# Kernel tuning notes

Hardware: AMD Instinct MI355X
Metric: run time of the kernel (lower is better)

Reference implementation:

```python
import jax, jax.numpy as jnp
import numpy as np

EMBED = 1024
HEADS = 16
HEAD_DIM = EMBED // HEADS
B, S = 2, 2048


def setup_inputs() -> dict:
    key = jax.random.key(0)
    ks = jax.random.split(key, 13)
    def lin(kw, kb):
        # torch nn.Linear default init: U(-1/sqrt(fan_in), 1/sqrt(fan_in))
        bound = 1.0 / np.sqrt(EMBED)
        W = jax.random.uniform(kw, (EMBED, EMBED), jnp.float32, -bound, bound)
        b = jax.random.uniform(kb, (EMBED,), jnp.float32, -bound, bound)
        return W, b
    Wq, bq = lin(ks[0], ks[1])
    Wk, bk = lin(ks[2], ks[3])
    Wv, bv = lin(ks[4], ks[5])
    Wo, bo = lin(ks[6], ks[7])
    return {
        "query": jax.random.normal(ks[8], (B, S, EMBED), jnp.float32),
        "key": jax.random.normal(ks[9], (B, S, EMBED), jnp.float32),
        "value": jax.random.normal(ks[10], (B, S, EMBED), jnp.float32),
        "mask": jax.random.randint(ks[11], (B, S, S), 0, 2, jnp.int32),
        "Wq": Wq, "bq": bq, "Wk": Wk, "bk": bk,
        "Wv": Wv, "bv": bv, "Wo": Wo, "bo": bo,
    }


def _split_heads(x):
    b, s, _ = x.shape
    return x.reshape(b, s, HEADS, HEAD_DIM).transpose(0, 2, 1, 3)  # [B,H,S,D]


def reference(query, key, value, mask, Wq, bq, Wk, bk, Wv, bv, Wo, bo):
    scaling = HEAD_DIM ** -0.5
    q = _split_heads(query @ Wq.T + bq) * scaling          # [B,H,Sq,D]
    k = _split_heads(key @ Wk.T + bk)                       # [B,H,Sk,D]
    v = _split_heads(value @ Wv.T + bv)                     # [B,H,Sk,D]
    scores = jnp.einsum('bhqd,bhkd->bhqk', q, k)            # [B,H,Sq,Sk]
    scores = jnp.where(mask[:, None, :, :] == 0, jnp.float32(-10000.0), scores)
    p = jax.nn.softmax(scores, axis=-1)
    x = jnp.einsum('bhqk,bhkd->bhqd', p, v)                 # [B,H,Sq,D]
    b, h, s, d = x.shape
    x = x.transpose(0, 2, 1, 3).reshape(b, s, h * d)
    return x @ Wo.T + bo
```

## Files before the change

kernel.cpp:

```cpp
#include <hip/hip_runtime.h>

#define EMBED 1024
#define HEADS 16
#define HDIM  64
#define BATCH 2
#define SEQ   2048
#define MTOT  (BATCH*SEQ)
#define LOG2E 1.4426950408889634f
#define QSCALE (0.125f * LOG2E)

typedef __attribute__((ext_vector_type(8)))  short short8;
typedef __attribute__((ext_vector_type(4)))  float f32x4;
typedef __attribute__((ext_vector_type(16))) float f32x16;

#define MFMA(a,b,c)   __builtin_amdgcn_mfma_f32_16x16x32_bf16(a,b,c,0,0,0)
#define MFMA32(a,b,c) __builtin_amdgcn_mfma_f32_32x32x16_bf16(a,b,c,0,0,0)

__device__ __forceinline__ ushort f2bf(float f) {
  union { float f; unsigned u; } v; v.f = f;
  unsigned u = v.u;
  unsigned r = u + 0x7fffu + ((u >> 16) & 1u);
  return (ushort)(r >> 16);
}
__device__ __forceinline__ unsigned packbf(float a, float b) {
  return (unsigned)f2bf(a) | ((unsigned)f2bf(b) << 16);
}
__device__ __forceinline__ unsigned cvtpk(float lo, float hi) {
  unsigned r;
  asm("v_cvt_pk_bf16_f32 %0, %1, %2" : "=v"(r) : "v"(lo), "v"(hi));
  return r;
}
__device__ __forceinline__ uint2 cvt4(float4 v) {
  uint2 r;
  asm("v_cvt_pk_bf16_f32 %0, %2, %3\n\t"
      "v_cvt_pk_bf16_f32 %1, %4, %5"
      : "=&v"(r.x), "=&v"(r.y)
      : "v"(v.x), "v"(v.y), "v"(v.z), "v"(v.w));
  return r;
}
__device__ __forceinline__ void gl_lds16(const ushort* g, ushort* l) {
  __builtin_amdgcn_global_load_lds(
      (const __attribute__((address_space(1))) unsigned*)g,
      (__attribute__((address_space(3))) unsigned*)l, 16, 0, 0);
}

__global__ __launch_bounds__(256) void prep(
    const float* __restrict__ s0, const float* __restrict__ s1, const float* __restrict__ s2,
    const float* __restrict__ s3, const float* __restrict__ s4, const float* __restrict__ s5,
    const float* __restrict__ s6, const int* __restrict__ mask,
    ushort* __restrict__ d0, ushort* __restrict__ d1, ushort* __restrict__ d2,
    ushort* __restrict__ d3, ushort* __restrict__ d4, ushort* __restrict__ d5,
    ushort* __restrict__ d6, ushort* __restrict__ mbits16)
{
  const int z = blockIdx.z;
  if (z == 7) {
    size_t i16 = ((size_t)blockIdx.x * 256 + threadIdx.x);
    if (i16 >= (size_t)BATCH * SEQ * SEQ / 16) return;
    const int4* m4 = reinterpret_cast<const int4*>(mask + i16 * 16);
    unsigned bits = 0;
    #pragma unroll
    for (int k = 0; k < 4; ++k) {
      int4 v = m4[k];
      bits |= (unsigned)(v.x != 0) << (4 * k);
      bits |= (unsigned)(v.y != 0) << (4 * k + 1);
      bits |= (unsigned)(v.z != 0) << (4 * k + 2);
      bits |= (unsigned)(v.w != 0) << (4 * k + 3);
    }
    mbits16[i16] = (ushort)bits;
    return;
  }
  const float* s; ushort* d;
  switch (z) {
    case 0: s = s0; d = d0; break;
    case 1: s = s1; d = d1; break;
    case 2: s = s2; d = d2; break;
    case 3: s = s3; d = d3; break;
    case 4: s = s4; d = d4; break;
    case 5: s = s5; d = d5; break;
    default: s = s6; d = d6; break;
  }
  const int nch = (z < 3) ? (MTOT * EMBED / 8) : (EMBED * EMBED / 8);
  int i = blockIdx.x * 256 + threadIdx.x;
  if (i >= nch) return;
  float4 a = reinterpret_cast<const float4*>(s)[2 * i];
  float4 b = reinterpret_cast<const float4*>(s)[2 * i + 1];
  uint2 lo = cvt4(a), hi = cvt4(b);
  reinterpret_cast<uint4*>(d)[i] = make_uint4(lo.x, lo.y, hi.x, hi.y);
}

__global__ __launch_bounds__(512, 6) void gemm_qkv32(
    const ushort* __restrict__ A0, const ushort* __restrict__ A1, const ushort* __restrict__ A2,
    const ushort* __restrict__ W0, const ushort* __restrict__ W1, const ushort* __restrict__ W2,
    const float* __restrict__ b0, const float* __restrict__ b1, const float* __restrict__ b2,
    ushort* __restrict__ oq, ushort* __restrict__ ok, ushort* __restrict__ ov)
{
  __shared__ __align__(16) ushort lds[2][2][4096];

  const int nwg = 768;
  int lin = blockIdx.x + (blockIdx.y << 3);
  int swz = (lin & 7) * (nwg >> 3) + (lin >> 3);
  const int z  = swz >> 8;
  const int r_ = swz & 255;
  const int n0 = (r_ & 7) << 7;
  const int m0 = (r_ >> 3) << 7;

  const ushort* __restrict__ A    = (z == 0) ? A0 : (z == 1) ? A1 : A2;
  const ushort* __restrict__ W    = (z == 0) ? W0 : (z == 1) ? W1 : W2;
  const float*  __restrict__ bias = (z == 0) ? b0 : (z == 1) ? b1 : b2;

  const int t = threadIdx.x;
  const int lane = t & 63;
  const int wid = t >> 6;
  const int wr = wid >> 2, wc = wid & 3;
  const int lr = lane & 15, qg = lane >> 4;

  const int srow = t >> 2;
  const int scol = ((((t & 3) - (srow >> 1)) & 3)) << 3;
  auto stage = [&](int buf, int k0) {
    gl_lds16(&A[(size_t)(m0 + srow) * EMBED + k0 + scol], &lds[buf][0][t * 8]);
    gl_lds16(&W[(size_t)(n0 + srow) * EMBED + k0 + scol], &lds[buf][1][t * 8]);
  };

  f32x4 acc[4][2] = {};

  stage(0, 0);
  asm volatile("s_waitcnt vmcnt(0)" ::: "memory");
  __syncthreads();

  for (int kt = 0; kt < 32; ++kt) {
    const int buf = kt & 1;
    if (kt < 31) stage(buf ^ 1, (kt + 1) * 32);

    short8 af[4], bfr[2];
    #pragma unroll
    for (int mi = 0; mi < 4; ++mi) {
      int row = wr * 64 + mi * 16 + lr;
      int sidx = (qg + (row >> 1)) & 3;
      af[mi] = *reinterpret_cast<const short8*>(&lds[buf][0][row * 32 + (sidx << 3)]);
    }
    #pragma unroll
    for (int ni = 0; ni < 2; ++ni) {
      int row = wc * 32 + ni * 16 + lr;
      int sidx = (qg + (row >> 1)) & 3;
      bfr[ni] = *reinterpret_cast<const short8*>(&lds[buf][1][row * 32 + (sidx << 3)]);
    }
    __builtin_amdgcn_s_setprio(1);
    #pragma unroll
    for (int mi = 0; mi < 4; ++mi)
      #pragma unroll
      for (int ni = 0; ni < 2; ++ni)
        acc[mi][ni] = MFMA(af[mi], bfr[ni], acc[mi][ni]);
    __builtin_amdgcn_s_setprio(0);

    if (kt < 31) {
      asm volatile("s_waitcnt vmcnt(0)" ::: "memory");
      __syncthreads();
    }
  }

  #pragma unroll
  for (int ni = 0; ni < 2; ++ni) {
    int ng = n0 + wc * 32 + ni * 16 + lr;
    float bv_ = bias[ng];
    int h = ng >> 6, d = ng & 63;
    #pragma unroll
    for (int mi = 0; mi < 4; ++mi) {
      #pragma unroll
      for (int r = 0; r < 4; ++r) {
        int mg = m0 + wr * 64 + mi * 16 + qg * 4 + r;
        float val = acc[mi][ni][r] + bv_;
        int bb = mg >> 11, s = mg & (SEQ - 1);
        int bh = bb * HEADS + h;
        if (z == 0)
          oq[((size_t)bh * SEQ + s) * HDIM + d] = f2bf(val * QSCALE);
        else if (z == 1)
          ok[((size_t)bh * SEQ + s) * HDIM + d] = f2bf(val);
        else {
          size_t addr = (((size_t)bh * 2 + (d >> 5)) * (SEQ / 32) + (s >> 5)) * 1024
                      + (size_t)(d & 31) * 32 + (s & 31);
          ov[addr] = f2bf(val);
        }
      }
    }
  }
}

__global__ __launch_bounds__(512, 4) void gemm_out128(
    const ushort* __restrict__ A0, const ushort* __restrict__ W0,
    const float* __restrict__ b0, float* __restrict__ of)
{
  __shared__ __align__(16) ushort lds[2][2][8192];

  const int nwg = 256;
  int lin = blockIdx.x + (blockIdx.y << 3);
  int swz = (lin & 7) * (nwg >> 3) + (lin >> 3);
  const int r_ = swz & 255;
  const int n0 = (r_ & 7) << 7;
  const int m0 = (r_ >> 3) << 7;

  const ushort* __restrict__ A = A0;
  const ushort* __restrict__ W = W0;
  const float*  __restrict__ bias = b0;

  const int t = threadIdx.x;
  const int lane = t & 63;
  const int wid = t >> 6;
  const int wr = wid >> 2, wc = wid & 3;
  const int lr = lane & 15, qg = lane >> 4;

  auto stage = [&](int buf, int k0) {
    #pragma unroll
    for (int it = 0; it < 2; ++it) {
      int idx = it * 512 + t;
      int row = idx >> 3;
      int col = ((idx & 7) ^ (row & 7)) << 3;
      gl_lds16(&A[(size_t)(m0 + row) * EMBED + k0 + col], &lds[buf][0][idx * 8]);
    }
    #pragma unroll
    for (int it = 0; it < 2; ++it) {
      int idx = it * 512 + t;
      int row = idx >> 3;
      int col = ((idx & 7) ^ (row & 7)) << 3;
      gl_lds16(&W[(size_t)(n0 + row) * EMBED + k0 + col], &lds[buf][1][idx * 8]);
    }
  };

  f32x4 acc[4][2] = {};

  stage(0, 0);
  asm volatile("s_waitcnt vmcnt(0)" ::: "memory");
  __syncthreads();

  for (int kt = 0; kt < 16; ++kt) {
    const int buf = kt & 1;
    if (kt < 15) stage(buf ^ 1, (kt + 1) * 64);

    #pragma unroll
    for (int ks = 0; ks < 2; ++ks) {
      short8 af[4], bfr[2];
      #pragma unroll
      for (int mi = 0; mi < 4; ++mi) {
        int row = wr * 64 + mi * 16 + lr;
        int cp = (ks * 4 + qg) ^ (row & 7);
        af[mi] = *reinterpret_cast<const short8*>(&lds[buf][0][row * 64 + (cp << 3)]);
      }
      #pragma unroll
      for (int ni = 0; ni < 2; ++ni) {
        int row = wc * 32 + ni * 16 + lr;
        int cp = (ks * 4 + qg) ^ (row & 7);
        bfr[ni] = *reinterpret_cast<const short8*>(&lds[buf][1][row * 64 + (cp << 3)]);
      }
      __builtin_amdgcn_s_setprio(1);
      #pragma unroll
      for (int mi = 0; mi < 4; ++mi)
        #pragma unroll
        for (int ni = 0; ni < 2; ++ni)
          acc[mi][ni] = MFMA(af[mi], bfr[ni], acc[mi][ni]);
      __builtin_amdgcn_s_setprio(0);
    }

    if (kt < 15) {
      asm volatile("s_waitcnt vmcnt(0)" ::: "memory");
      __syncthreads();
    }
  }

  #pragma unroll
  for (int ni = 0; ni < 2; ++ni) {
    int ng = n0 + wc * 32 + ni * 16 + lr;
    float bv_ = bias[ng];
    #pragma unroll
    for (int mi = 0; mi < 4; ++mi) {
      #pragma unroll
      for (int r = 0; r < 4; ++r) {
        int mg = m0 + wr * 64 + mi * 16 + qg * 4 + r;
        of[(size_t)mg * EMBED + ng] = acc[mi][ni][r] + bv_;
      }
    }
  }
}

__global__ __launch_bounds__(256, 2) void attn(
    const ushort* __restrict__ qws, const ushort* __restrict__ kws,
    const ushort* __restrict__ vws, const unsigned* __restrict__ mbits,
    ushort* __restrict__ xws)
{
  const int t = threadIdx.x;
  const int wid = t >> 6;
  const int l = t & 63;
  const int q31 = l & 31;
  const int h = l >> 5;

  const int L = blockIdx.x;
  const int j = L >> 3;
  const int bh = ((L & 7) << 2) + (j >> 4);
  const int q0 = (j & 15) << 7;
  const int b = bh >> 4, head = bh & 15;

  __shared__ __align__(16) ushort lds[9216];

  const int qrow = q0 + wid * 32 + q31;
  const ushort* qp = qws + ((size_t)bh * SEQ + qrow) * HDIM + 8 * h;
  short8 qf[4];
  #pragma unroll
  for (int s = 0; s < 4; ++s)
    qf[s] = *reinterpret_cast<const short8*>(qp + 16 * s);

  const int rp = (q31 & 19) | ((q31 & 4) << 1) | ((q31 & 8) >> 1);

  int koff[4];
  #pragma unroll
  for (int i = 0; i < 4; ++i)
    koff[i] = rp * 64 + (((h + 2 * i) ^ (rp & 7)) << 3);
  int voff[2][2];
  #pragma unroll
  for (int sb = 0; sb < 2; ++sb)
    #pragma unroll
    for (int jj = 0; jj < 2; ++jj)
      voff[sb][jj] = sb * 1024 + q31 * 32 + (((h + 2 * jj) ^ ((q31 >> 1) & 3)) << 3);

  const ushort* ksb = kws + (size_t)bh * SEQ * HDIM
                    + ((t >> 3) << 6) + (((t & 7) ^ ((t >> 3) & 7)) << 3);
  const int vsub = t >> 7, vd = (t >> 2) & 31, vc = t & 3;
  const ushort* vsb = vws + (((size_t)bh * 2 + vsub) << 16)
                    + vd * 32 + ((vc ^ ((vd >> 1) & 3)) << 3);
  ushort* kd0 = lds + t * 8;
  ushort* vd0 = lds + 2048 + t * 8;

  const unsigned* mp = mbits + (size_t)(b * SEQ + qrow) * (SEQ / 32);

  f32x16 accT[2] = {};
  float ls0 = 0.f, ls1 = 0.f, ls2 = 0.f, ls3 = 0.f;

  auto STAGE = [&](int tile, int bb) {
    gl_lds16(ksb + (size_t)tile * 2048, kd0 + bb);
    gl_lds16(vsb + (size_t)tile * 1024, vd0 + bb);
  };

  auto COMP = [&](int bb, unsigned mwc) {
    const ushort* kb = lds + bb;
    const ushort* vb = lds + bb + 2048;
    short8 kf0 = *reinterpret_cast<const short8*>(kb + koff[0]);
    short8 kf1 = *reinterpret_cast<const short8*>(kb + koff[1]);
    short8 kf2 = *reinterpret_cast<const short8*>(kb + koff[2]);
    short8 kf3 = *reinterpret_cast<const short8*>(kb + koff[3]);
    __builtin_amdgcn_s_setprio(1);
    f32x16 s = {};
    s = MFMA32(kf0, qf[0], s);
    s = MFMA32(kf1, qf[1], s);
    s = MFMA32(kf2, qf[2], s);
    s = MFMA32(kf3, qf[3], s);
    __builtin_amdgcn_s_setprio(0);

    short8 vf0 = *reinterpret_cast<const short8*>(vb + voff[0][0]);
    short8 vf1 = *reinterpret_cast<const short8*>(vb + voff[0][1]);
    short8 vf2 = *reinterpret_cast<const short8*>(vb + voff[1][0]);
    short8 vf3 = *reinterpret_cast<const short8*>(vb + voff[1][1]);

    unsigned msh = mwc >> (8 * h);
    union U { unsigned u[4]; short8 s8; } p0u, p1u;
    #pragma unroll
    for (int i = 0; i < 8; ++i) {
      const int r0 = 2 * i, r1 = 2 * i + 1;
      float e0 = ((msh >> ((r0 & 7) + 16 * (r0 >> 3))) & 1u) ? __builtin_amdgcn_exp2f(s[r0]) : 0.0f;
      float e1 = ((msh >> ((r1 & 7) + 16 * (r1 >> 3))) & 1u) ? __builtin_amdgcn_exp2f(s[r1]) : 0.0f;
      if ((i & 3) == 0) ls0 += e0 + e1;
      else if ((i & 3) == 1) ls1 += e0 + e1;
      else if ((i & 3) == 2) ls2 += e0 + e1;
      else ls3 += e0 + e1;
      if (i < 4) p0u.u[i] = cvtpk(e0, e1);
      else       p1u.u[i - 4] = cvtpk(e0, e1);
    }

    __builtin_amdgcn_s_setprio(1);
    accT[0] = MFMA32(vf0, p0u.s8, accT[0]);
    accT[0] = MFMA32(vf1, p1u.s8, accT[0]);
    accT[1] = MFMA32(vf2, p0u.s8, accT[1]);
    accT[1] = MFMA32(vf3, p1u.s8, accT[1]);
    __builtin_amdgcn_s_setprio(0);
  };

  unsigned mw = *mp; ++mp;
  STAGE(0, 0);
  asm volatile("s_waitcnt vmcnt(0)" ::: "memory");
  __syncthreads();

  #pragma unroll 1
  for (int it = 0; it < 32; ++it) {
    STAGE(2 * it + 1, 4096);
    unsigned mn = *mp; ++mp;
    COMP(0, mw);
    asm volatile("s_waitcnt vmcnt(0)" ::: "memory");
    __syncthreads();
    mw = mn;
    if (it < 31) STAGE(2 * it + 2, 0);
    mn = *mp; ++mp;
    COMP(4096, mw);
    asm volatile("s_waitcnt vmcnt(0)" ::: "memory");
    __syncthreads();
    mw = mn;
  }

  float lsum = (ls0 + ls1) + (ls2 + ls3);
  float lrow = lsum + __shfl_xor(lsum, 32);
  float inv = 1.0f / lrow;

  ushort* xb = lds + wid * 2304;
  #pragma unroll
  for (int nb = 0; nb < 2; ++nb)
    #pragma unroll
    for (int rg = 0; rg < 4; ++rg) {
      int dbase = 32 * nb + 8 * rg + 4 * h;
      uint2 pk = make_uint2(
          packbf(accT[nb][4 * rg] * inv,     accT[nb][4 * rg + 1] * inv),
          packbf(accT[nb][4 * rg + 2] * inv, accT[nb][4 * rg + 3] * inv));
      *reinterpret_cast<uint2*>(&xb[q31 * 72 + dbase]) = pk;
    }
  asm volatile("" ::: "memory");
  #pragma unroll
  for (int pp = 0; pp < 4; ++pp) {
    int row = pp * 8 + (l >> 3);
    int col = (l & 7) * 8;
    short8 xv = *reinterpret_cast<const short8*>(&xb[row * 72 + col]);
    *reinterpret_cast<short8*>(
        &xws[((size_t)b * SEQ + q0 + wid * 32 + row) * EMBED + head * HDIM + col]) = xv;
  }
}

extern "C" void kernel_launch(void* const* d_in, const int* in_sizes, int n_in,
                              void* d_out, int out_size, void* d_ws, size_t ws_size,
                              hipStream_t stream) {
  (void)in_sizes; (void)n_in; (void)out_size; (void)ws_size;
  const float* query = (const float*)d_in[0];
  const float* key   = (const float*)d_in[1];
  const float* value = (const float*)d_in[2];
  const int*   mask  = (const int*)d_in[3];
  const float* Wq = (const float*)d_in[4];  const float* bq = (const float*)d_in[5];
  const float* Wk = (const float*)d_in[6];  const float* bk = (const float*)d_in[7];
  const float* Wv = (const float*)d_in[8];  const float* bv = (const float*)d_in[9];
  const float* Wo = (const float*)d_in[10]; const float* bo = (const float*)d_in[11];
  float* out = (float*)d_out;

  const size_t NQKV = (size_t)BATCH * HEADS * SEQ * HDIM;
  const size_t NW   = (size_t)EMBED * EMBED;
  ushort* qws = (ushort*)d_ws;
  ushort* kws = qws + NQKV;
  ushort* vws = kws + NQKV;
  ushort* xws = vws + NQKV;
  unsigned* mbits = (unsigned*)(xws + NQKV);
  ushort* aqb = (ushort*)(mbits + (size_t)BATCH * SEQ * SEQ / 32);
  ushort* akb = aqb + NQKV;
  ushort* avb = akb + NQKV;
  ushort* wqb = avb + NQKV;
  ushort* wkb = wqb + NW;
  ushort* wvb = wkb + NW;
  ushort* wob = wvb + NW;

  prep<<<dim3(2048, 1, 8), 256, 0, stream>>>(
      query, key, value, Wq, Wk, Wv, Wo, mask,
      aqb, akb, avb, wqb, wkb, wvb, wob, (ushort*)mbits);

  gemm_qkv32<<<dim3(8, 96), 512, 0, stream>>>(
      aqb, akb, avb, wqb, wkb, wvb, bq, bk, bv, qws, kws, vws);

  attn<<<dim3(512), 256, 0, stream>>>(qws, kws, vws, mbits, xws);

  gemm_out128<<<dim3(8, 32), 512, 0, stream>>>(xws, wob, bo, out);
}
```

Before: 142.9 us.

## Split attention over two KV halves with separate merge kernel

```diff
diff --git a/kernel.cpp b/kernel.cpp
--- a/kernel.cpp
+++ b/kernel.cpp
@@ -280,10 +280,10 @@
   }
 }
 
-__global__ __launch_bounds__(256, 2) void attn(
+__global__ __launch_bounds__(256, 4) void attn_part(
     const ushort* __restrict__ qws, const ushort* __restrict__ kws,
     const ushort* __restrict__ vws, const unsigned* __restrict__ mbits,
-    ushort* __restrict__ xws)
+    float* __restrict__ pacc, float* __restrict__ plsum)
 {
   const int t = threadIdx.x;
   const int wid = t >> 6;
@@ -293,11 +293,15 @@
 
   const int L = blockIdx.x;
   const int j = L >> 3;
-  const int bh = ((L & 7) << 2) + (j >> 4);
-  const int q0 = (j & 15) << 7;
-  const int b = bh >> 4, head = bh & 15;
-
-  __shared__ __align__(16) ushort lds[9216];
+  const int bh = ((L & 7) << 2) + (j >> 5);
+  const int rem = j & 31;
+  const int qt = rem >> 1;
+  const int half = rem & 1;
+  const int q0 = qt << 7;
+  const int kv0 = half << 10;
+  const int b = bh >> 4;
+
+  __shared__ __align__(16) ushort lds[8192];
 
   const int qrow = q0 + wid * 32 + q31;
   const ushort* qp = qws + ((size_t)bh * SEQ + qrow) * HDIM + 8 * h;
@@ -319,15 +323,15 @@
     for (int jj = 0; jj < 2; ++jj)
       voff[sb][jj] = sb * 1024 + q31 * 32 + (((h + 2 * jj) ^ ((q31 >> 1) & 3)) << 3);
 
-  const ushort* ksb = kws + (size_t)bh * SEQ * HDIM
+  const ushort* ksb = kws + (size_t)bh * SEQ * HDIM + (size_t)kv0 * HDIM
                     + ((t >> 3) << 6) + (((t & 7) ^ ((t >> 3) & 7)) << 3);
   const int vsub = t >> 7, vd = (t >> 2) & 31, vc = t & 3;
-  const ushort* vsb = vws + (((size_t)bh * 2 + vsub) << 16)
+  const ushort* vsb = vws + (((size_t)bh * 2 + vsub) << 16) + (kv0 >> 5) * 1024
                     + vd * 32 + ((vc ^ ((vd >> 1) & 3)) << 3);
   ushort* kd0 = lds + t * 8;
   ushort* vd0 = lds + 2048 + t * 8;
 
-  const unsigned* mp = mbits + (size_t)(b * SEQ + qrow) * (SEQ / 32);
+  const unsigned* mp = mbits + (size_t)(b * SEQ + qrow) * (SEQ / 32) + (kv0 >> 5);
 
   f32x16 accT[2] = {};
   float ls0 = 0.f, ls1 = 0.f, ls2 = 0.f, ls3 = 0.f;
@@ -386,14 +390,14 @@
   __syncthreads();
 
   #pragma unroll 1
-  for (int it = 0; it < 32; ++it) {
+  for (int it = 0; it < 16; ++it) {
     STAGE(2 * it + 1, 4096);
     unsigned mn = *mp; ++mp;
     COMP(0, mw);
     asm volatile("s_waitcnt vmcnt(0)" ::: "memory");
     __syncthreads();
     mw = mn;
-    if (it < 31) STAGE(2 * it + 2, 0);
+    if (it < 15) STAGE(2 * it + 2, 0);
     mn = *mp; ++mp;
     COMP(4096, mw);
     asm volatile("s_waitcnt vmcnt(0)" ::: "memory");
@@ -403,17 +407,65 @@
 
   float lsum = (ls0 + ls1) + (ls2 + ls3);
   float lrow = lsum + __shfl_xor(lsum, 32);
-  float inv = 1.0f / lrow;
-
-  ushort* xb = lds + wid * 2304;
+
+  size_t pidx = ((((size_t)half * 32 + bh) * 16 + qt) * 4 + wid) * 64 + l;
+  float4* pd = reinterpret_cast<float4*>(pacc + pidx * 32);
+  #pragma unroll
+  for (int k = 0; k < 4; ++k)
+    pd[k] = make_float4(accT[0][4 * k], accT[0][4 * k + 1],
+                        accT[0][4 * k + 2], accT[0][4 * k + 3]);
+  #pragma unroll
+  for (int k = 0; k < 4; ++k)
+    pd[4 + k] = make_float4(accT[1][4 * k], accT[1][4 * k + 1],
+                            accT[1][4 * k + 2], accT[1][4 * k + 3]);
+  if (h == 0)
+    plsum[((((size_t)half * 32 + bh) * 16 + qt) * 4 + wid) * 32 + q31] = lrow;
+}
+
+__global__ __launch_bounds__(256) void attn_merge(
+    const float* __restrict__ pacc, const float* __restrict__ plsum,
+    ushort* __restrict__ xws)
+{
+  const int B_ = blockIdx.x;
+  const int bh = B_ >> 4;
+  const int qt = B_ & 15;
+  const int t = threadIdx.x;
+  const int wid = t >> 6;
+  const int l = t & 63;
+  const int q31 = l & 31;
+  const int h = l >> 5;
+  const int q0 = qt << 7;
+  const int b = bh >> 4, head = bh & 15;
+
+  __shared__ __align__(16) ushort xball[4 * 2304];
+
+  size_t i0 = ((((size_t)0 * 32 + bh) * 16 + qt) * 4 + wid) * 64 + l;
+  size_t i1 = ((((size_t)1 * 32 + bh) * 16 + qt) * 4 + wid) * 64 + l;
+  const float4* p0 = reinterpret_cast<const float4*>(pacc + i0 * 32);
+  const float4* p1 = reinterpret_cast<const float4*>(pacc + i1 * 32);
+
+  float l0 = plsum[((((size_t)0 * 32 + bh) * 16 + qt) * 4 + wid) * 32 + q31];
+  float l1 = plsum[((((size_t)1 * 32 + bh) * 16 + qt) * 4 + wid) * 32 + q31];
+  float inv = 1.0f / (l0 + l1);
+
+  float v[32];
+  #pragma unroll
+  for (int k = 0; k < 8; ++k) {
+    float4 a = p0[k], c = p1[k];
+    v[4 * k]     = (a.x + c.x) * inv;
+    v[4 * k + 1] = (a.y + c.y) * inv;
+    v[4 * k + 2] = (a.z + c.z) * inv;
+    v[4 * k + 3] = (a.w + c.w) * inv;
+  }
+
+  ushort* xb = xball + wid * 2304;
   #pragma unroll
   for (int nb = 0; nb < 2; ++nb)
     #pragma unroll
     for (int rg = 0; rg < 4; ++rg) {
       int dbase = 32 * nb + 8 * rg + 4 * h;
-      uint2 pk = make_uint2(
-          packbf(accT[nb][4 * rg] * inv,     accT[nb][4 * rg + 1] * inv),
-          packbf(accT[nb][4 * rg + 2] * inv, accT[nb][4 * rg + 3] * inv));
+      uint2 pk = make_uint2(packbf(v[16 * nb + 4 * rg],     v[16 * nb + 4 * rg + 1]),
+                            packbf(v[16 * nb + 4 * rg + 2], v[16 * nb + 4 * rg + 3]));
       *reinterpret_cast<uint2*>(&xb[q31 * 72 + dbase]) = pk;
     }
   asm volatile("" ::: "memory");
@@ -448,13 +500,15 @@
   ushort* vws = kws + NQKV;
   ushort* xws = vws + NQKV;
   unsigned* mbits = (unsigned*)(xws + NQKV);
-  ushort* aqb = (ushort*)(mbits + (size_t)BATCH * SEQ * SEQ / 32);
-  ushort* akb = aqb + NQKV;
-  ushort* avb = akb + NQKV;
-  ushort* wqb = avb + NQKV;
+  ushort* wqb = (ushort*)(mbits + (size_t)BATCH * SEQ * SEQ / 32);
   ushort* wkb = wqb + NW;
   ushort* wvb = wkb + NW;
   ushort* wob = wvb + NW;
+  ushort* aqb = wob + NW;
+  ushort* akb = aqb + NQKV;
+  ushort* avb = akb + NQKV;
+  float* pacc  = (float*)aqb;
+  float* plsum = pacc + (size_t)1024 * 256 * 32;
 
   prep<<<dim3(2048, 1, 8), 256, 0, stream>>>(
       query, key, value, Wq, Wk, Wv, Wo, mask,
@@ -463,7 +517,9 @@
   gemm_qkv32<<<dim3(8, 96), 512, 0, stream>>>(
       aqb, akb, avb, wqb, wkb, wvb, bq, bk, bv, qws, kws, vws);
 
-  attn<<<dim3(512), 256, 0, stream>>>(qws, kws, vws, mbits, xws);
+  attn_part<<<dim3(1024), 256, 0, stream>>>(qws, kws, vws, mbits, pacc, plsum);
+
+  attn_merge<<<dim3(512), 256, 0, stream>>>(pacc, plsum, xws);
 
   gemm_out128<<<dim3(8, 32), 512, 0, stream>>>(xws, wob, bo, out);
 }
```

Result: slower. 154.0 us (+7.8%).
